# Kernel tuning notes

Hardware: AMD Instinct MI355X
Metric: run time of the kernel (lower is better)

## Reference

```python
import jax, jax.numpy as jnp
import numpy as np

N, D_IN, H, E, L = 8192, 512, 256, 262144, 2
LN_EPS = 1e-5


def _unique_edges(rng, n, e):
    # sample unique (src,tgt) pairs so scatter-set semantics are well-defined
    flat = np.unique(rng.integers(0, n * n, size=int(e * 1.2)))
    rng.shuffle(flat)
    flat = flat[:e]
    assert flat.shape[0] == e
    return np.stack([flat // n, flat % n]).astype(np.int64)


def setup_inputs() -> dict:
    key = jax.random.key(0)
    ks = jax.random.split(key, 8)
    rng = np.random.default_rng(0)
    inv = lambda fan: 1.0 / np.sqrt(fan)
    return {
        "node_features": jax.random.normal(ks[0], (N, D_IN), jnp.float32),
        "edge_index": jnp.asarray(_unique_edges(rng, N, E)),
        "W_in": jax.random.uniform(ks[1], (H, D_IN), jnp.float32, -inv(D_IN), inv(D_IN)),
        "b_in": jnp.zeros((H,), jnp.float32),
        "W_gat": jax.random.uniform(ks[2], (L, H, H), jnp.float32, -inv(H), inv(H)),
        "a_gat": jax.random.uniform(ks[3], (L, 2 * H), jnp.float32, -inv(2 * H), inv(2 * H)),
        "ln_g": jnp.ones((L, H), jnp.float32),
        "ln_b": jnp.zeros((L, H), jnp.float32),
        "W_pool": jax.random.uniform(ks[4], (1, H), jnp.float32, -inv(H), inv(H)),
        "b_pool": jnp.zeros((1,), jnp.float32),
    }


def _layer_norm(x, g, b):
    mu = x.mean(-1, keepdims=True)
    var = ((x - mu) ** 2).mean(-1, keepdims=True)
    return (x - mu) * jax.lax.rsqrt(var + LN_EPS) * g + b


def reference(node_features, edge_index, W_in, b_in, W_gat, a_gat, ln_g, ln_b, W_pool, b_pool):
    src, tgt = edge_index[0], edge_index[1]
    n = node_features.shape[0]
    h = node_features @ W_in.T + b_in  # (N, H)
    nl = W_gat.shape[0]
    for l in range(nl):
        hw = h @ W_gat[l].T  # (N, H)
        # attention score per edge: attn([h_src || h_tgt]) with LeakyReLU(0.2)
        e = hw[src] @ a_gat[l, :H] + hw[tgt] @ a_gat[l, H:]  # (E,)
        e = jnp.where(e > 0, e, 0.2 * e)
        # faithful to torch: dense NxN with zeros at non-edges, full-row softmax
        alpha = jnp.zeros((n, n), h.dtype).at[src, tgt].set(e)
        alpha = jax.nn.softmax(alpha, axis=-1)
        h_new = alpha @ hw  # (N, H)  (dropout is eval-mode identity)
        h = _layer_norm(h + h_new, ln_g[l], ln_b[l])
        h = jax.nn.elu(h)
    gate = jax.nn.sigmoid(h @ W_pool.T + b_pool)  # (N, 1)
    graph_emb = (gate * h).sum(axis=0)  # (H,)
    return h, graph_emb
```

## Files before the change

### kernel.cpp

```cpp
#include <hip/hip_runtime.h>
#include <hip/hip_bf16.h>
#include <stdint.h>

#define NN 8192
#define DIN 512
#define HH 256
#define EE 262144
#define CAP 96
#define LN_EPS 1e-5f

typedef __attribute__((ext_vector_type(8))) short bf16x8;
typedef __attribute__((ext_vector_type(4))) short s16x4;
typedef __attribute__((ext_vector_type(4))) float f32x4;

__device__ __forceinline__ short f2bf_bits(float x) {
    __hip_bfloat16 b = __float2bfloat16(x);
    return __builtin_bit_cast(short, b);
}
__device__ __forceinline__ float bf2f(short s) {
    uint32_t u = ((uint32_t)(uint16_t)s) << 16;
    return __builtin_bit_cast(float, u);
}
__device__ __forceinline__ void load16_lds(const void* g, void* l) {
    __builtin_amdgcn_global_load_lds((const __attribute__((address_space(1))) uint32_t*)g,
                                     (__attribute__((address_space(3))) uint32_t*)l, 16, 0, 0);
}

#define NW1 (HH * DIN)
#define NW2 (2 * HH * HH)
#define ZCOUNT (2 * (2 * NN + HH) + NN)
__global__ __launch_bounds__(256) void prep(const float* __restrict__ W_in, __hip_bfloat16* __restrict__ Wb_in,
                                            const float* __restrict__ W_gat, __hip_bfloat16* __restrict__ Wgb,
                                            float* __restrict__ zbase, float* __restrict__ emb) {
    int gtid = blockIdx.x * 256 + threadIdx.x;
    if (gtid < ZCOUNT) ((int*)zbase)[gtid] = 0;
    if (gtid < HH) emb[gtid] = 0.f;
    int q = gtid * 4;
    const float* x;
    __hip_bfloat16* y;
    int b;
    if (q < NW1) { x = W_in; y = Wb_in; b = q; }
    else { x = W_gat; y = Wgb; b = q - NW1; }
    float4 v = *(const float4*)(x + b);
    s16x4 s = { f2bf_bits(v.x), f2bf_bits(v.y), f2bf_bits(v.z), f2bf_bits(v.w) };
    *(s16x4*)((short*)y + b) = s;
}

#define GEMM_BLOCKS 512
__global__ __launch_bounds__(256) void gemm_in_fill(const float* __restrict__ X,
                                                    const __hip_bfloat16* __restrict__ B,
                                                    const float* __restrict__ bias,
                                                    __hip_bfloat16* __restrict__ Cb,
                                                    const int* __restrict__ src, const int* __restrict__ tgt,
                                                    int* __restrict__ cnt, int* __restrict__ buck) {
    __shared__ __hip_bfloat16 As[64 * 32];
    __shared__ __hip_bfloat16 Bs[64 * 32];
    const int bid = blockIdx.x;
    if (bid >= GEMM_BLOCKS) {
        int k = ((bid - GEMM_BLOCKS) * 256 + threadIdx.x) * 2;
        int2 sv = *(const int2*)(src + k);
        int2 tv = *(const int2*)(tgt + k);
        int p = atomicAdd(&cnt[sv.x], 1);
        if (p < CAP) buck[sv.x * CAP + p] = tv.x;
        p = atomicAdd(&cnt[sv.y], 1);
        if (p < CAP) buck[sv.y * CAP + p] = tv.y;
        return;
    }
    const int tid = threadIdx.x;
    const int row0 = (bid >> 2) * 64, col0 = (bid & 3) * 64;
    const int w = tid >> 6, l = tid & 63;
    const int quad = l >> 4, r = l & 15;
    const int mh = (w & 1) * 32, nh = (w >> 1) * 32;
    f32x4 acc[2][2] = {};

    const int srow = tid >> 2, scol = (tid & 3) * 8;
    const float* gA = X + (size_t)(row0 + srow) * DIN + scol;
    const __hip_bfloat16* gB = B + (size_t)(col0 + srow) * DIN + scol;
    __hip_bfloat16* lB = &Bs[tid * 8];

    for (int k0 = 0; k0 < DIN; k0 += 32) {
        float4 a0 = *(const float4*)(gA + k0);
        float4 a1 = *(const float4*)(gA + k0 + 4);
        load16_lds(gB + k0, lB);
        bf16x8 av;
        av[0] = f2bf_bits(a0.x); av[1] = f2bf_bits(a0.y);
        av[2] = f2bf_bits(a0.z); av[3] = f2bf_bits(a0.w);
        av[4] = f2bf_bits(a1.x); av[5] = f2bf_bits(a1.y);
        av[6] = f2bf_bits(a1.z); av[7] = f2bf_bits(a1.w);
        *(bf16x8*)&As[tid * 8] = av;
        __syncthreads();
        bf16x8 aF[2], bF[2];
#pragma unroll
        for (int mi = 0; mi < 2; mi++)
            aF[mi] = *(const bf16x8*)&As[(mh + mi * 16 + r) * 32 + quad * 8];
#pragma unroll
        for (int ni = 0; ni < 2; ni++)
            bF[ni] = *(const bf16x8*)&Bs[(nh + ni * 16 + r) * 32 + quad * 8];
#pragma unroll
        for (int mi = 0; mi < 2; mi++)
#pragma unroll
            for (int ni = 0; ni < 2; ni++)
                acc[mi][ni] = __builtin_amdgcn_mfma_f32_16x16x32_bf16(aF[mi], bF[ni], acc[mi][ni], 0, 0, 0);
        __syncthreads();
    }

#pragma unroll
    for (int mi = 0; mi < 2; mi++)
#pragma unroll
        for (int ni = 0; ni < 2; ni++) {
            int gcol = col0 + nh + ni * 16 + r;
            float bv = bias[gcol];
#pragma unroll
            for (int reg = 0; reg < 4; reg++) {
                int grow = row0 + mh + mi * 16 + quad * 4 + reg;
                Cb[(size_t)grow * HH + gcol] = __float2bfloat16(acc[mi][ni][reg] + bv);
            }
        }
}

__global__ __launch_bounds__(256) void gemm_bb_score(const __hip_bfloat16* __restrict__ A,
                                                     const __hip_bfloat16* __restrict__ B,
                                                     __hip_bfloat16* __restrict__ Cb,
                                                     const float* __restrict__ ag1,
                                                     const float* __restrict__ ag2,
                                                     float* __restrict__ s1, float* __restrict__ s2,
                                                     float* __restrict__ St,
                                                     int Nc, int K) {
    __shared__ __hip_bfloat16 As[64 * 32];
    __shared__ __hip_bfloat16 Bs[64 * 32];
    const int tid = threadIdx.x;
    const int row0 = blockIdx.y * 64, col0 = blockIdx.x * 64;
    const int w = tid >> 6, l = tid & 63;
    const int quad = l >> 4, r = l & 15;
    const int mh = (w & 1) * 32, nh = (w >> 1) * 32;
    f32x4 acc[2][2] = {};

    const int srow = tid >> 2, scol = (tid & 3) * 8;
    const __hip_bfloat16* gA = A + (size_t)(row0 + srow) * K + scol;
    const __hip_bfloat16* gB = B + (size_t)(col0 + srow) * K + scol;
    __hip_bfloat16* lA = &As[tid * 8];
    __hip_bfloat16* lB = &Bs[tid * 8];

    for (int k0 = 0; k0 < K; k0 += 32) {
        load16_lds(gA + k0, lA);
        load16_lds(gB + k0, lB);
        __syncthreads();
        bf16x8 aF[2], bF[2];
#pragma unroll
        for (int mi = 0; mi < 2; mi++)
            aF[mi] = *(const bf16x8*)&As[(mh + mi * 16 + r) * 32 + quad * 8];
#pragma unroll
        for (int ni = 0; ni < 2; ni++)
            bF[ni] = *(const bf16x8*)&Bs[(nh + ni * 16 + r) * 32 + quad * 8];
#pragma unroll
        for (int mi = 0; mi < 2; mi++)
#pragma unroll
            for (int ni = 0; ni < 2; ni++)
                acc[mi][ni] = __builtin_amdgcn_mfma_f32_16x16x32_bf16(aF[mi], bF[ni], acc[mi][ni], 0, 0, 0);
        __syncthreads();
    }

#pragma unroll
    for (int mi = 0; mi < 2; mi++)
#pragma unroll
        for (int ni = 0; ni < 2; ni++) {
            int gcol = col0 + nh + ni * 16 + r;
#pragma unroll
            for (int reg = 0; reg < 4; reg++) {
                int grow = row0 + mh + mi * 16 + quad * 4 + reg;
                Cb[(size_t)grow * Nc + gcol] = __float2bfloat16(acc[mi][ni][reg]);
            }
        }

    float a1v[2], a2v[2];
#pragma unroll
    for (int ni = 0; ni < 2; ni++) {
        int gcol = col0 + nh + ni * 16 + r;
        a1v[ni] = ag1[gcol];
        a2v[ni] = ag2[gcol];
    }
#pragma unroll
    for (int mi = 0; mi < 2; mi++)
#pragma unroll
        for (int reg = 0; reg < 4; reg++) {
            float p1 = acc[mi][0][reg] * a1v[0] + acc[mi][1][reg] * a1v[1];
            float p2 = acc[mi][0][reg] * a2v[0] + acc[mi][1][reg] * a2v[1];
#pragma unroll
            for (int off = 1; off <= 8; off <<= 1) {
                p1 += __shfl_xor(p1, off);
                p2 += __shfl_xor(p2, off);
            }
            if (r == 0) {
                int grow = row0 + mh + mi * 16 + quad * 4 + reg;
                atomicAdd(&s1[grow], p1);
                atomicAdd(&s2[grow], p2);
            }
        }
#pragma unroll
    for (int ni = 0; ni < 2; ni++) {
        float pS = 0.f;
#pragma unroll
        for (int mi = 0; mi < 2; mi++)
#pragma unroll
            for (int reg = 0; reg < 4; reg++) pS += acc[mi][ni][reg];
        pS += __shfl_xor(pS, 16);
        pS += __shfl_xor(pS, 32);
        if (quad == 0) atomicAdd(&St[col0 + nh + ni * 16 + r], pS);
    }
}

__global__ __launch_bounds__(256) void gat_row(const __hip_bfloat16* __restrict__ hprev,
                                               const __hip_bfloat16* __restrict__ hw,
                                               const int* __restrict__ cnt, const int* __restrict__ buck,
                                               const float* __restrict__ s1, const float* __restrict__ s2,
                                               const float* __restrict__ St,
                                               const float* __restrict__ lng, const float* __restrict__ lnb,
                                               const float* __restrict__ W_pool, const float* __restrict__ b_pool,
                                               float* __restrict__ houtf, __hip_bfloat16* __restrict__ houtb,
                                               float* __restrict__ emb, int last) {
    __shared__ float emb_s[4][HH];
    const int wv = threadIdx.x >> 6, lane = threadIdx.x & 63;
    const int half = lane >> 5, sl = lane & 31;
    const int i = blockIdx.x * 4 + wv;
    const int deg = cnt[i];
    const int base = i * CAP;
    const float s1i = s1[i];
    const short* hws = (const short*)hw;

    float u[8] = {};
    float lsum = 0.f;

    for (int kb = 0; kb < deg; kb += 64) {
        int k = kb + lane;
        float wk = 0.f;
        int ck = 0;
        if (k < deg) {
            int j = buck[base + k];
            float e = s1i + s2[j];
            e = e > 0.f ? e : 0.2f * e;
            wk = __expf(e) - 1.f;
            ck = j;
        }
        lsum += wk;
        int nb = min(64, deg - kb);
        int npair = (nb + 1) >> 1;
#pragma unroll 4
        for (int jj = 0; jj < npair; jj++) {
            float wj = __shfl(wk, 2 * jj + half);
            int cj = __shfl(ck, 2 * jj + half);
            bf16x8 hv = *(const bf16x8*)(hws + (size_t)cj * HH + 8 * sl);
#pragma unroll
            for (int q = 0; q < 8; q++) u[q] += wj * bf2f(hv[q]);
        }
    }
#pragma unroll
    for (int q = 0; q < 8; q++) u[q] += __shfl_xor(u[q], 32);
#pragma unroll
    for (int off = 32; off; off >>= 1) lsum += __shfl_xor(lsum, off);
    const float inv = 1.f / ((float)NN + lsum);

    float4 Sa = *(const float4*)(St + 8 * sl);
    float4 Sb = *(const float4*)(St + 8 * sl + 4);
    float Sts[8] = { Sa.x, Sa.y, Sa.z, Sa.w, Sb.x, Sb.y, Sb.z, Sb.w };
    bf16x8 hp = *(const bf16x8*)((const short*)hprev + (size_t)i * HH + 8 * sl);
    float x[8];
    float part = 0.f;
#pragma unroll
    for (int q = 0; q < 8; q++) { x[q] = bf2f(hp[q]) + (Sts[q] + u[q]) * inv; part += x[q]; }
#pragma unroll
    for (int off = 16; off; off >>= 1) part += __shfl_xor(part, off);
    float mu = part * (1.f / HH);
    float d[8];
    float vs = 0.f;
#pragma unroll
    for (int q = 0; q < 8; q++) { d[q] = x[q] - mu; vs += d[q] * d[q]; }
#pragma unroll
    for (int off = 16; off; off >>= 1) vs += __shfl_xor(vs, off);
    float rstd = rsqrtf(vs * (1.f / HH) + LN_EPS);
    float4 ga = *(const float4*)(lng + 8 * sl);
    float4 gb = *(const float4*)(lng + 8 * sl + 4);
    float4 ba = *(const float4*)(lnb + 8 * sl);
    float4 bb = *(const float4*)(lnb + 8 * sl + 4);
    float gg[8] = { ga.x, ga.y, ga.z, ga.w, gb.x, gb.y, gb.z, gb.w };
    float bv[8] = { ba.x, ba.y, ba.z, ba.w, bb.x, bb.y, bb.z, bb.w };
    float y[8];
#pragma unroll
    for (int q = 0; q < 8; q++) {
        float t = d[q] * rstd * gg[q] + bv[q];
        y[q] = t > 0.f ? t : __expf(t) - 1.f;
    }

    const int co = 8 * sl + 4 * half;
    if (houtb) {
        s16x4 yv;
#pragma unroll
        for (int q = 0; q < 4; q++) yv[q] = f2bf_bits(y[4 * half + q]);
        *(s16x4*)((short*)houtb + (size_t)i * HH + co) = yv;
    }
    if (houtf) {
        float4 yf = { y[4 * half], y[4 * half + 1], y[4 * half + 2], y[4 * half + 3] };
        *(float4*)(houtf + (size_t)i * HH + co) = yf;
    }

    if (last) {
        float4 wa = *(const float4*)(W_pool + 8 * sl);
        float4 wb = *(const float4*)(W_pool + 8 * sl + 4);
        float wp[8] = { wa.x, wa.y, wa.z, wa.w, wb.x, wb.y, wb.z, wb.w };
        float p = 0.f;
#pragma unroll
        for (int q = 0; q < 8; q++) p += y[q] * wp[q];
#pragma unroll
        for (int off = 16; off; off >>= 1) p += __shfl_xor(p, off);
        float g = 1.f / (1.f + __expf(-(p + b_pool[0])));
#pragma unroll
        for (int q = 0; q < 4; q++) emb_s[wv][co + q] = g * y[4 * half + q];
        __syncthreads();
        int c = threadIdx.x;
        float s = emb_s[0][c] + emb_s[1][c] + emb_s[2][c] + emb_s[3][c];
        atomicAdd(&emb[c], s);
    }
}

extern "C" void kernel_launch(void* const* d_in, const int* in_sizes, int n_in,
                              void* d_out, int out_size, void* d_ws, size_t ws_size,
                              hipStream_t stream) {
    const float* X      = (const float*)d_in[0];
    const int*   ei     = (const int*)d_in[1];
    const float* W_in   = (const float*)d_in[2];
    const float* b_in   = (const float*)d_in[3];
    const float* W_gat  = (const float*)d_in[4];
    const float* a_gat  = (const float*)d_in[5];
    const float* ln_g   = (const float*)d_in[6];
    const float* ln_b   = (const float*)d_in[7];
    const float* W_pool = (const float*)d_in[8];
    const float* b_pool = (const float*)d_in[9];
    float* out = (float*)d_out;

    __hip_bfloat16* hb    = (__hip_bfloat16*)d_ws;
    __hip_bfloat16* hwb   = hb + (size_t)NN * HH;
    __hip_bfloat16* Wb_in = hwb + (size_t)NN * HH;
    __hip_bfloat16* Wgb   = Wb_in + (size_t)HH * DIN;
    float* zbase = (float*)(Wgb + (size_t)2 * HH * HH);
    float* s1_0 = zbase;
    float* s2_0 = s1_0 + NN;
    float* St_0 = s2_0 + NN;
    float* s1_1 = St_0 + HH;
    float* s2_1 = s1_1 + NN;
    float* St_1 = s2_1 + NN;
    int* cnt  = (int*)(St_1 + HH);
    int* buck = (int*)(cnt + NN);

    const int* src = ei;
    const int* tgt = ei + EE;
    float* emb = out + (size_t)NN * HH;

    prep<<<256, 256, 0, stream>>>(W_in, Wb_in, W_gat, Wgb, zbase, emb);

    gemm_in_fill<<<GEMM_BLOCKS + EE / 512, 256, 0, stream>>>(X, Wb_in, b_in, hb, src, tgt, cnt, buck);

    for (int ll = 0; ll < 2; ll++) {
        float* s1 = ll ? s1_1 : s1_0;
        float* s2 = ll ? s2_1 : s2_0;
        float* St = ll ? St_1 : St_0;
        const float* ag = a_gat + (size_t)ll * 2 * HH;
        gemm_bb_score<<<dim3(HH / 64, NN / 64), 256, 0, stream>>>(hb, Wgb + (size_t)ll * HH * HH, hwb,
                                                                  ag, ag + HH, s1, s2, St, HH, HH);
        gat_row<<<NN / 4, 256, 0, stream>>>(hb, hwb, cnt, buck, s1, s2, St,
                                            ln_g + (size_t)ll * HH, ln_b + (size_t)ll * HH,
                                            W_pool, b_pool,
                                            (ll == 1) ? out : nullptr,
                                            (ll == 0) ? hb : nullptr,
                                            emb, ll);
    }
}
```

Baseline: 209.4 us.

## Bucket edges per source by target band for locality in gather

Edge buckets are split per source node into four target-index bands, each with its own counter and capacity. The gather then walks the bands in order, so neighbour row reads are grouped by target range, which may improve cache locality. Score computation moves into the pair loop and replaces the per-chunk shuffles. The prep grid is doubled to zero the larger counter array, and the weight-conversion stores are guarded. Per-band capacity of 40 could overflow for skewed graphs, and recomputing weights per pair duplicates some loads.

```diff
diff --git a/kernel.cpp b/kernel.cpp
--- a/kernel.cpp
+++ b/kernel.cpp
@@ -6,7 +6,8 @@
 #define DIN 512
 #define HH 256
 #define EE 262144
-#define CAP 96
+#define NBAND 4
+#define CAPB 40
 #define LN_EPS 1e-5f
 
 typedef __attribute__((ext_vector_type(8))) short bf16x8;
@@ -28,7 +29,7 @@
 
 #define NW1 (HH * DIN)
 #define NW2 (2 * HH * HH)
-#define ZCOUNT (2 * (2 * NN + HH) + NN)
+#define ZCOUNT (2 * (2 * NN + HH) + NN * NBAND)
 __global__ __launch_bounds__(256) void prep(const float* __restrict__ W_in, __hip_bfloat16* __restrict__ Wb_in,
                                             const float* __restrict__ W_gat, __hip_bfloat16* __restrict__ Wgb,
                                             float* __restrict__ zbase, float* __restrict__ emb) {
@@ -36,14 +37,16 @@
     if (gtid < ZCOUNT) ((int*)zbase)[gtid] = 0;
     if (gtid < HH) emb[gtid] = 0.f;
     int q = gtid * 4;
-    const float* x;
-    __hip_bfloat16* y;
-    int b;
-    if (q < NW1) { x = W_in; y = Wb_in; b = q; }
-    else { x = W_gat; y = Wgb; b = q - NW1; }
-    float4 v = *(const float4*)(x + b);
-    s16x4 s = { f2bf_bits(v.x), f2bf_bits(v.y), f2bf_bits(v.z), f2bf_bits(v.w) };
-    *(s16x4*)((short*)y + b) = s;
+    if (q < NW1 + NW2) {
+        const float* x;
+        __hip_bfloat16* y;
+        int b;
+        if (q < NW1) { x = W_in; y = Wb_in; b = q; }
+        else { x = W_gat; y = Wgb; b = q - NW1; }
+        float4 v = *(const float4*)(x + b);
+        s16x4 s = { f2bf_bits(v.x), f2bf_bits(v.y), f2bf_bits(v.z), f2bf_bits(v.w) };
+        *(s16x4*)((short*)y + b) = s;
+    }
 }
 
 #define GEMM_BLOCKS 512
@@ -60,10 +63,12 @@
         int k = ((bid - GEMM_BLOCKS) * 256 + threadIdx.x) * 2;
         int2 sv = *(const int2*)(src + k);
         int2 tv = *(const int2*)(tgt + k);
-        int p = atomicAdd(&cnt[sv.x], 1);
-        if (p < CAP) buck[sv.x * CAP + p] = tv.x;
-        p = atomicAdd(&cnt[sv.y], 1);
-        if (p < CAP) buck[sv.y * CAP + p] = tv.y;
+        int b1 = sv.x * NBAND + (tv.x >> 11);
+        int p = atomicAdd(&cnt[b1], 1);
+        if (p < CAPB) buck[b1 * CAPB + p] = tv.x;
+        int b2 = sv.y * NBAND + (tv.y >> 11);
+        p = atomicAdd(&cnt[b2], 1);
+        if (p < CAPB) buck[b2 * CAPB + p] = tv.y;
         return;
     }
     const int tid = threadIdx.x;
@@ -222,32 +227,31 @@
     const int wv = threadIdx.x >> 6, lane = threadIdx.x & 63;
     const int half = lane >> 5, sl = lane & 31;
     const int i = blockIdx.x * 4 + wv;
-    const int deg = cnt[i];
-    const int base = i * CAP;
     const float s1i = s1[i];
     const short* hws = (const short*)hw;
 
+    int4 cv = *(const int4*)(cnt + i * NBAND);
+    int degs[NBAND] = { min(cv.x, CAPB), min(cv.y, CAPB), min(cv.z, CAPB), min(cv.w, CAPB) };
+
     float u[8] = {};
     float lsum = 0.f;
 
-    for (int kb = 0; kb < deg; kb += 64) {
-        int k = kb + lane;
-        float wk = 0.f;
-        int ck = 0;
-        if (k < deg) {
-            int j = buck[base + k];
-            float e = s1i + s2[j];
-            e = e > 0.f ? e : 0.2f * e;
-            wk = __expf(e) - 1.f;
-            ck = j;
-        }
-        lsum += wk;
-        int nb = min(64, deg - kb);
-        int npair = (nb + 1) >> 1;
+    for (int bd = 0; bd < NBAND; bd++) {
+        const int dego = degs[bd];
+        const int* bk = buck + (size_t)(i * NBAND + bd) * CAPB;
+        const int npair = (dego + 1) >> 1;
 #pragma unroll 4
         for (int jj = 0; jj < npair; jj++) {
-            float wj = __shfl(wk, 2 * jj + half);
-            int cj = __shfl(ck, 2 * jj + half);
+            int eidx = 2 * jj + half;
+            int cj = 0;
+            float wj = 0.f;
+            if (eidx < dego) {
+                cj = bk[eidx];
+                float e = s1i + s2[cj];
+                e = e > 0.f ? e : 0.2f * e;
+                wj = __expf(e) - 1.f;
+            }
+            lsum += wj;
             bf16x8 hv = *(const bf16x8*)(hws + (size_t)cj * HH + 8 * sl);
 #pragma unroll
             for (int q = 0; q < 8; q++) u[q] += wj * bf2f(hv[q]);
@@ -255,8 +259,7 @@
     }
 #pragma unroll
     for (int q = 0; q < 8; q++) u[q] += __shfl_xor(u[q], 32);
-#pragma unroll
-    for (int off = 32; off; off >>= 1) lsum += __shfl_xor(lsum, off);
+    lsum += __shfl_xor(lsum, 32);
     const float inv = 1.f / ((float)NN + lsum);
 
     float4 Sa = *(const float4*)(St + 8 * sl);
@@ -348,13 +351,13 @@
     float* s2_1 = s1_1 + NN;
     float* St_1 = s2_1 + NN;
     int* cnt  = (int*)(St_1 + HH);
-    int* buck = (int*)(cnt + NN);
+    int* buck = (int*)(cnt + (size_t)NN * NBAND);
 
     const int* src = ei;
     const int* tgt = ei + EE;
     float* emb = out + (size_t)NN * HH;
 
-    prep<<<256, 256, 0, stream>>>(W_in, Wb_in, W_gat, Wgb, zbase, emb);
+    prep<<<512, 256, 0, stream>>>(W_in, Wb_in, W_gat, Wgb, zbase, emb);
 
     gemm_in_fill<<<GEMM_BLOCKS + EE / 512, 256, 0, stream>>>(X, Wb_in, b_in, hb, src, tgt, cnt, buck);
 
```

Result: slower. 238.2 us (+13.7%).
